# Optimization experiments

Measured on AMD Instinct MI355X. Metric: run time of the kernel, lower is better.

Reference implementation:

```python
import jax, jax.numpy as jnp
import numpy as np

B, T, F, H = 4, 2048, 512, 8
DK = F // H


def setup_inputs() -> dict:
    key = jax.random.key(0)
    ks = jax.random.split(key, 12)
    s = 1.0 / np.sqrt(F)
    return {
        "query": jax.random.normal(ks[0], (B, T, F), jnp.float32),
        "key": jax.random.normal(ks[1], (B, T, F), jnp.float32),
        "value": jax.random.normal(ks[2], (B, T, F), jnp.float32),
        "attn_mask": jax.random.randint(ks[3], (B, 1, T), 0, 2, jnp.int32),
        "Wq": jax.random.uniform(ks[4], (F, F), jnp.float32, -s, s),
        "bq": jax.random.uniform(ks[5], (F,), jnp.float32, -s, s),
        "Wk": jax.random.uniform(ks[6], (F, F), jnp.float32, -s, s),
        "bk": jax.random.uniform(ks[7], (F,), jnp.float32, -s, s),
        "Wv": jax.random.uniform(ks[8], (F, F), jnp.float32, -s, s),
        "bv": jax.random.uniform(ks[9], (F,), jnp.float32, -s, s),
        "Wo": jax.random.uniform(ks[10], (F, F), jnp.float32, -s, s),
        "bo": jax.random.uniform(ks[11], (F,), jnp.float32, -s, s),
    }


def reference(query, key, value, attn_mask, Wq, bq, Wk, bk, Wv, bv, Wo, bo):
    b = query.shape[0]
    # QKV projections -> (b, h, t, d_k)
    q = (query @ Wq.T + bq).reshape(b, -1, H, DK).transpose(0, 2, 1, 3)
    k = (key @ Wk.T + bk).reshape(b, -1, H, DK).transpose(0, 2, 1, 3)
    v = (value @ Wv.T + bv).reshape(b, -1, H, DK).transpose(0, 2, 1, 3)
    scores = jnp.einsum("bhqd,bhkd->bhqk", q, k) / np.sqrt(DK)
    # mask (b,1,t2) -> (b,1,1,t2); masked where mask == 0
    m = (attn_mask[:, None, :, :] == 0)
    min_val = jnp.finfo(scores.dtype).min
    scores = jnp.where(m, min_val, scores)
    attn = jnp.where(m, 0.0, jax.nn.softmax(scores, axis=-1))
    # dropout is identity in eval mode
    x = jnp.einsum("bhqk,bhkd->bhqd", attn, v)
    x = x.transpose(0, 2, 1, 3).reshape(b, -1, H * DK)
    return x @ Wo.T + bo
```

## Files before the change

### kernel.cpp

```cpp
#include <hip/hip_runtime.h>
#include <hip/hip_bf16.h>
#include <stdint.h>

#define B_ 4
#define T_ 2048
#define F_ 512
#define H_ 8
#define DK_ 64
#define BT_ (B_*T_)

typedef short bf16x8 __attribute__((ext_vector_type(8)));
typedef short s16x4 __attribute__((ext_vector_type(4)));
typedef float f32x4 __attribute__((ext_vector_type(4)));
typedef float f32x16 __attribute__((ext_vector_type(16)));

__device__ __forceinline__ unsigned short f2bf(float f) {
  union { float f; unsigned u; } v; v.f = f;
  return (unsigned short)((v.u + 0x7fffu + ((v.u >> 16) & 1u)) >> 16);
}

__device__ __forceinline__ unsigned cvtpk(float lo, float hi) {
  unsigned w;
  asm("v_cvt_pk_bf16_f32 %0, %1, %2" : "=v"(w) : "v"(lo), "v"(hi));
  return w;
}

__device__ __forceinline__ void gload_lds16(const void* g, void* l) {
  __builtin_amdgcn_global_load_lds((const __attribute__((address_space(1))) void*)g,
                                   (__attribute__((address_space(3))) void*)l, 16, 0, 0);
}

__global__ void convert_scan(const float* __restrict__ wq, const float* __restrict__ wk,
                             const float* __restrict__ wv, const float* __restrict__ wo,
                             const int* __restrict__ mask,
                             unsigned short* __restrict__ dst, int* __restrict__ invidx,
                             int* __restrict__ nbuf) {
  const int seg = blockIdx.y;
  const int tid = threadIdx.x;
  if (seg == 4) {
    if (blockIdx.x >= 4) return;
    const int b = blockIdx.x;
    __shared__ int cnt[256];
    const int base = b * T_ + tid * 8;
    int4 a = *(const int4*)(mask + base);
    int4 d = *(const int4*)(mask + base + 4);
    int m[8] = {a.x, a.y, a.z, a.w, d.x, d.y, d.z, d.w};
    int c = 0;
#pragma unroll
    for (int i = 0; i < 8; ++i) c += (m[i] != 0);
    cnt[tid] = c;
    __syncthreads();
    for (int off = 1; off < 256; off <<= 1) {
      int v = (tid >= off) ? cnt[tid - off] : 0;
      __syncthreads();
      cnt[tid] += v;
      __syncthreads();
    }
    int excl = cnt[tid] - c;
#pragma unroll
    for (int i = 0; i < 8; ++i)
      if (m[i]) { invidx[b * T_ + excl] = tid * 8 + i; ++excl; }
    if (tid == 255) nbuf[b] = cnt[255];
    return;
  }
  const float* src = seg == 0 ? wq : (seg == 1 ? wk : (seg == 2 ? wv : wo));
  unsigned short* out = dst + (size_t)seg * F_ * F_;
  const int idx = (blockIdx.x * 256 + tid) * 8;
  float4 a = *(const float4*)(src + idx);
  float4 b = *(const float4*)(src + idx + 4);
  union { unsigned w[4]; bf16x8 v; } t;
  t.w[0] = cvtpk(a.x, a.y); t.w[1] = cvtpk(a.z, a.w);
  t.w[2] = cvtpk(b.x, b.y); t.w[3] = cvtpk(b.z, b.w);
  *(bf16x8*)(out + idx) = t.v;
}

__global__ __launch_bounds__(256, 3) void gemm_qkv(
    const float* __restrict__ qin, const float* __restrict__ kin, const float* __restrict__ vin,
    const unsigned short* __restrict__ Wbase,
    const float* __restrict__ bq, const float* __restrict__ bk, const float* __restrict__ bv,
    const int* __restrict__ invidx, const int* __restrict__ nbuf,
    unsigned short* __restrict__ projq, unsigned short* __restrict__ kc,
    unsigned short* __restrict__ vt, float qscale) {
  const int id0 = blockIdx.x;
  const int id = (id0 & 7) * 96 + (id0 >> 3);
  const int p = id >> 8, l = id & 255;
  const int tid = threadIdx.x;
  const int wid = tid >> 6, lane = tid & 63;
  const int lr = lane & 15, lg = lane >> 4;
  const int wr = wid >> 1, wc = wid & 1;
  const int n0 = (l & 3) * 128;

  const float* Af;
  const float* bias;
  float sc = 1.0f;
  int obase, j0 = 0, b = 0, nb = T_;
  if (p == 0) {
    obase = (l >> 2) * 128;
    Af = qin; bias = bq; sc = qscale;
  } else {
    b = l >> 6;
    j0 = ((l >> 2) & 15) * 128;
    nb = nbuf[b];
    if (j0 >= ((nb + 63) & ~63)) return;
    obase = b * T_ + j0;
    Af = (p == 1) ? kin : vin;
    bias = (p == 1) ? bk : bv;
  }
  const unsigned short* W = Wbase + (size_t)p * F_ * F_;

  __shared__ __align__(16) unsigned short As[128 * 64];
  __shared__ __align__(16) unsigned short Bs[128 * 64];

  int srcrow[4];
#pragma unroll
  for (int i = 0; i < 4; ++i) {
    const int r = (i * 256 + tid) >> 3;
    if (p == 0) srcrow[i] = obase + r;
    else {
      int j = j0 + r;
      if (j >= nb) j = nb - 1;
      srcrow[i] = b * T_ + invidx[b * T_ + j];
    }
  }

  float4 aR[4][2];
  auto loadA = [&](int k0) {
#pragma unroll
    for (int i = 0; i < 4; ++i) {
      const int s = (i * 256 + tid) & 7;
      const float* sp = Af + (size_t)srcrow[i] * F_ + k0 + s * 8;
      aR[i][0] = *(const float4*)sp;
      aR[i][1] = *(const float4*)(sp + 4);
    }
  };
  auto writeA = [&]() {
#pragma unroll
    for (int i = 0; i < 4; ++i) {
      const int ch = i * 256 + tid;
      const int r = ch >> 3, s = ch & 7;
      union { unsigned w[4]; bf16x8 v; } t;
      t.w[0] = cvtpk(aR[i][0].x, aR[i][0].y); t.w[1] = cvtpk(aR[i][0].z, aR[i][0].w);
      t.w[2] = cvtpk(aR[i][1].x, aR[i][1].y); t.w[3] = cvtpk(aR[i][1].z, aR[i][1].w);
      *(bf16x8*)&As[r * 64 + ((s ^ (r & 7)) * 8)] = t.v;
    }
  };
  auto stageB = [&](int k0) {
#pragma unroll
    for (int i = 0; i < 4; ++i) {
      const int ch = i * 256 + tid;
      const int r = ch >> 3, s = ch & 7;
      gload_lds16(W + (size_t)(n0 + r) * F_ + k0 + ((s ^ (r & 7)) * 8),
                  &Bs[(i * 256 + wid * 64) * 8]);
    }
  };

  f32x4 acc[4][4] = {};
  loadA(0);
  for (int k0 = 0; k0 < F_; k0 += 64) {
    stageB(k0);
    writeA();
    __syncthreads();
    if (k0 + 64 < F_) loadA(k0 + 64);

#pragma unroll
    for (int kk = 0; kk < 2; ++kk) {
      bf16x8 af[4], bf[4];
      const int slotA = (kk * 4 + lg) ^ (lr & 7);
#pragma unroll
      for (int m = 0; m < 4; ++m)
        af[m] = *(const bf16x8*)&As[(wr * 64 + m * 16 + lr) * 64 + slotA * 8];
#pragma unroll
      for (int n = 0; n < 4; ++n)
        bf[n] = *(const bf16x8*)&Bs[(wc * 64 + n * 16 + lr) * 64 + slotA * 8];
#pragma unroll
      for (int m = 0; m < 4; ++m)
#pragma unroll
        for (int n = 0; n < 4; ++n)
          acc[m][n] = __builtin_amdgcn_mfma_f32_16x16x32_bf16(af[m], bf[n], acc[m][n], 0, 0, 0);
    }
    __syncthreads();
  }

  if (p == 2) {
#pragma unroll
    for (int n = 0; n < 4; ++n) {
      const int col = n0 + wc * 64 + n * 16 + lr;
      const float bvv = bias[col];
      unsigned short* vrow = vt + ((size_t)(b * 8 + (col >> 6)) * 64 + (col & 63)) * T_;
#pragma unroll
      for (int m = 0; m < 4; ++m) {
        const int kv = j0 + wr * 64 + m * 16 + lg * 4;
        union { unsigned short u[4]; s16x4 v; } ov;
#pragma unroll
        for (int j = 0; j < 4; ++j) ov.u[j] = f2bf(acc[m][n][j] + bvv);
        *(s16x4*)(vrow + kv) = ov.v;
      }
    }
  } else {
    unsigned short* outp = (p == 0) ? projq : kc;
#pragma unroll
    for (int n = 0; n < 4; ++n) {
      const int col = n0 + wc * 64 + n * 16 + lr;
      const float bvv = bias[col];
#pragma unroll
      for (int m = 0; m < 4; ++m) {
        const int rbase = obase + wr * 64 + m * 16 + lg * 4;
#pragma unroll
        for (int j = 0; j < 4; ++j)
          outp[(size_t)(rbase + j) * F_ + col] = f2bf((acc[m][n][j] + bvv) * sc);
      }
    }
  }
}

__global__ __launch_bounds__(256, 3) void gemm_out(
    const unsigned short* __restrict__ Abf, const unsigned short* __restrict__ W,
    const float* __restrict__ bias, float* __restrict__ outf) {
  const int id0 = blockIdx.x;
  const int l = (id0 & 7) * 64 + (id0 >> 3);
  const int m0 = (l >> 2) * 64, n0 = (l & 3) * 128;
  const int tid = threadIdx.x;
  const int wid = tid >> 6, lane = tid & 63;
  const int lr = lane & 15, lg = lane >> 4;
  const int wr = wid >> 1, wc = wid & 1;

  __shared__ __align__(16) unsigned short As[64 * 64];
  __shared__ __align__(16) unsigned short Bs[128 * 64];

  auto stage = [&](int k0) {
#pragma unroll
    for (int i = 0; i < 2; ++i) {
      const int ch = i * 256 + tid;
      const int r = ch >> 3, s = ch & 7;
      gload_lds16(Abf + (size_t)(m0 + r) * F_ + k0 + ((s ^ (r & 7)) * 8),
                  &As[(i * 256 + wid * 64) * 8]);
    }
#pragma unroll
    for (int i = 0; i < 4; ++i) {
      const int ch = i * 256 + tid;
      const int r = ch >> 3, s = ch & 7;
      gload_lds16(W + (size_t)(n0 + r) * F_ + k0 + ((s ^ (r & 7)) * 8),
                  &Bs[(i * 256 + wid * 64) * 8]);
    }
  };

  f32x4 acc[2][4] = {};
  for (int k0 = 0; k0 < F_; k0 += 64) {
    stage(k0);
    __syncthreads();
#pragma unroll
    for (int kk = 0; kk < 2; ++kk) {
      bf16x8 af[2], bf[4];
      const int slotA = (kk * 4 + lg) ^ (lr & 7);
#pragma unroll
      for (int m = 0; m < 2; ++m)
        af[m] = *(const bf16x8*)&As[(wr * 32 + m * 16 + lr) * 64 + slotA * 8];
#pragma unroll
      for (int n = 0; n < 4; ++n)
        bf[n] = *(const bf16x8*)&Bs[(wc * 64 + n * 16 + lr) * 64 + slotA * 8];
#pragma unroll
      for (int m = 0; m < 2; ++m)
#pragma unroll
        for (int n = 0; n < 4; ++n)
          acc[m][n] = __builtin_amdgcn_mfma_f32_16x16x32_bf16(af[m], bf[n], acc[m][n], 0, 0, 0);
    }
    __syncthreads();
  }

#pragma unroll
  for (int n = 0; n < 4; ++n) {
    const int col = n0 + wc * 64 + n * 16 + lr;
    const float bvv = bias[col];
#pragma unroll
    for (int m = 0; m < 2; ++m) {
      const int rbase = m0 + wr * 32 + m * 16 + lg * 4;
#pragma unroll
      for (int j = 0; j < 4; ++j)
        outf[(size_t)(rbase + j) * F_ + col] = acc[m][n][j] + bvv;
    }
  }
}

__global__ __launch_bounds__(256, 2) void attn_kernel(
    const unsigned short* __restrict__ Qp,
    const unsigned short* __restrict__ Kp,
    const unsigned short* __restrict__ Vt,
    const int* __restrict__ nbuf,
    unsigned short* __restrict__ X) {
  const int tid = threadIdx.x, wid = tid >> 6, lane = tid & 63;
  const int la = lane & 31, hi = lane >> 5;
  const int id = blockIdx.x;
  const int swz = (id & 7) * 64 + (id >> 3);
  const int bh = swz >> 4, qb = swz & 15;
  const int b = bh >> 3, h = bh & 7;
  const int qrow = qb * 128 + wid * 32 + la;
  const int nb = nbuf[b];
  const int nt = (nb + 127) >> 7;

  __shared__ __align__(16) unsigned short Ks[2][128 * 64];
  __shared__ __align__(16) unsigned short Vs[2][64 * 128];

  bf16x8 qf[4];
#pragma unroll
  for (int kk = 0; kk < 4; ++kk)
    qf[kk] = *(const bf16x8*)(Qp + (size_t)(b * T_ + qrow) * F_ + h * DK_ + kk * 16 + hi * 8);

  f32x16 oacc[2] = {};
  float lrun = 0.0f;

  auto stage = [&](int buf, int kv0) {
#pragma unroll
    for (int i = 0; i < 4; ++i) {
      const int ch = i * 256 + tid;
      const int r = ch >> 3, s = ch & 7;
      gload_lds16(Kp + (size_t)(b * T_ + kv0 + r) * F_ + h * DK_ + ((s ^ (r & 7)) * 8),
                  &Ks[buf][(i * 256 + wid * 64) * 8]);
      const int d = ch >> 4, s2 = ch & 15;
      gload_lds16(Vt + ((size_t)bh * DK_ + d) * T_ + kv0 + ((s2 ^ (d & 15)) * 8),
                  &Vs[buf][(i * 256 + wid * 64) * 8]);
    }
  };

  if (nt > 0) {
    stage(0, 0);
    __syncthreads();

    for (int t = 0; t < nt; ++t) {
      const int cur = t & 1;
      const int kv0 = t * 128;
      if (t < nt - 1) stage(cur ^ 1, kv0 + 128);

      f32x16 sb[4];
      __builtin_amdgcn_s_setprio(1);
#pragma unroll
      for (int n = 0; n < 4; ++n) {
        bf16x8 kf[4];
#pragma unroll
        for (int kk = 0; kk < 4; ++kk)
          kf[kk] = *(const bf16x8*)&Ks[cur][(n * 32 + la) * 64 + ((((kk << 1) | hi) ^ (la & 7)) * 8)];
        f32x16 s = {};
#pragma unroll
        for (int kk = 0; kk < 4; ++kk)
          s = __builtin_amdgcn_mfma_f32_32x32x16_bf16(kf[kk], qf[kk], s, 0, 0, 0);
        sb[n] = s;
      }
      __builtin_amdgcn_s_setprio(0);

      if (kv0 + 128 > nb) {
        const int kvb = kv0 + 4 * hi;
#pragma unroll
        for (int n = 0; n < 4; ++n)
#pragma unroll
          for (int r = 0; r < 16; ++r) {
            const int kv = kvb + n * 32 + (r & 3) + 8 * (r >> 2);
            if (kv >= nb) sb[n][r] = -__builtin_inff();
          }
      }
#pragma unroll
      for (int n = 0; n < 4; ++n)
#pragma unroll
        for (int r = 0; r < 16; ++r)
          sb[n][r] = __builtin_amdgcn_exp2f(sb[n][r]);

      float sm[16];
#pragma unroll
      for (int r = 0; r < 16; ++r)
        sm[r] = (sb[0][r] + sb[1][r]) + (sb[2][r] + sb[3][r]);
#pragma unroll
      for (int st = 8; st > 0; st >>= 1)
#pragma unroll
        for (int r = 0; r < st; ++r) sm[r] += sm[r + st];
      lrun += sm[0] + __shfl_xor(sm[0], 32, 64);

      unsigned lowr[4][2][2], uppr[4][2][2];
#pragma unroll
      for (int n = 0; n < 4; ++n)
#pragma unroll
        for (int gg = 0; gg < 2; ++gg)
#pragma unroll
          for (int hh = 0; hh < 2; ++hh) {
            unsigned xE = cvtpk(sb[n][4 * (2 * gg) + 2 * hh], sb[n][4 * (2 * gg) + 2 * hh + 1]);
            unsigned xO = cvtpk(sb[n][4 * (2 * gg + 1) + 2 * hh], sb[n][4 * (2 * gg + 1) + 2 * hh + 1]);
            asm("v_permlane32_swap_b32 %0, %1" : "+v"(xE), "+v"(xO));
            lowr[n][gg][hh] = xE;
            uppr[n][gg][hh] = xO;
          }

#pragma unroll
      for (int kt = 0; kt < 8; ++kt) {
        const int n = kt >> 1, gg = kt & 1;
        union { unsigned w[4]; bf16x8 v; } pf;
        pf.w[0] = lowr[n][gg][0]; pf.w[1] = lowr[n][gg][1];
        pf.w[2] = uppr[n][gg][0]; pf.w[3] = uppr[n][gg][1];
        __builtin_amdgcn_s_setprio(1);
#pragma unroll
        for (int m = 0; m < 2; ++m) {
          const int d = m * 32 + la;
          bf16x8 vfr = *(const bf16x8*)&Vs[cur][d * 128 + ((((kt << 1) | hi) ^ (d & 15)) * 8)];
          oacc[m] = __builtin_amdgcn_mfma_f32_32x32x16_bf16(vfr, pf.v, oacc[m], 0, 0, 0);
        }
        __builtin_amdgcn_s_setprio(0);
      }
      __syncthreads();
    }
  }

  const float inv = 1.0f / fmaxf(lrun, 1e-37f);
#pragma unroll
  for (int m = 0; m < 2; ++m)
#pragma unroll
    for (int g = 0; g < 4; ++g) {
      union { unsigned short u[4]; s16x4 v; } ov;
#pragma unroll
      for (int j = 0; j < 4; ++j) ov.u[j] = f2bf(oacc[m][4 * g + j] * inv);
      *(s16x4*)(X + (size_t)(b * T_ + qrow) * F_ + h * DK_ + m * 32 + 8 * g + 4 * hi) = ov.v;
    }
}

extern "C" void kernel_launch(void* const* d_in, const int* in_sizes, int n_in,
                              void* d_out, int out_size, void* d_ws, size_t ws_size,
                              hipStream_t stream) {
  const float* q  = (const float*)d_in[0];
  const float* k  = (const float*)d_in[1];
  const float* v  = (const float*)d_in[2];
  const int* mask = (const int*)d_in[3];
  const float* Wq = (const float*)d_in[4];
  const float* bq = (const float*)d_in[5];
  const float* Wk = (const float*)d_in[6];
  const float* bk = (const float*)d_in[7];
  const float* Wv = (const float*)d_in[8];
  const float* bv = (const float*)d_in[9];
  const float* Wo = (const float*)d_in[10];
  const float* bo = (const float*)d_in[11];
  float* out = (float*)d_out;

  unsigned short* ws = (unsigned short*)d_ws;
  unsigned short* wts   = ws;
  unsigned short* projq = wts + (size_t)4 * F_ * F_;
  unsigned short* kc    = projq + (size_t)BT_ * F_;
  unsigned short* vt    = kc + (size_t)BT_ * F_;
  unsigned short* xbuf  = vt + (size_t)BT_ * F_;
  int* invidx  = (int*)(xbuf + (size_t)BT_ * F_);
  int* nbuf    = invidx + BT_;

  const float kQScale = 0.18033688011112042f;

  convert_scan<<<dim3(128, 5, 1), 256, 0, stream>>>(
      Wq, Wk, Wv, Wo, mask, wts, invidx, nbuf);
  gemm_qkv<<<dim3(768, 1, 1), 256, 0, stream>>>(
      q, k, v, wts, bq, bk, bv, invidx, nbuf, projq, kc, vt, kQScale);
  attn_kernel<<<dim3(512, 1, 1), 256, 0, stream>>>(
      projq, kc, vt, nbuf, xbuf);
  gemm_out<<<dim3(512, 1, 1), 256, 0, stream>>>(
      xbuf, wts + (size_t)3 * F_ * F_, bo, out);
}
```

Measured before the change: 70.18 us.

## Use 512-thread attention blocks with triple-buffered KV and MFMA row sums

The attention kernel now runs 256 blocks of 8 waves, each covering 256 query rows, so every staged K/V tile is shared by twice as many waves. K/V staging moves from double to triple buffering with explicit vmcnt waits and one barrier per iteration, letting loads run two tiles ahead. The softmax denominator is now computed by an extra MFMA against a ones vector instead of VALU reductions and a shuffle. The cost is fewer blocks, more LDS per block (about 96KB), one extra MFMA per k-step, and reliance on hand-counted vmcnt values for correctness.

After: 68.68 us. 2.1% less time.

```diff
diff --git a/kernel.cpp b/kernel.cpp
--- a/kernel.cpp
+++ b/kernel.cpp
@@ -281,7 +281,7 @@
   }
 }
 
-__global__ __launch_bounds__(256, 2) void attn_kernel(
+__global__ __launch_bounds__(512, 1) void attn_kernel(
     const unsigned short* __restrict__ Qp,
     const unsigned short* __restrict__ Kp,
     const unsigned short* __restrict__ Vt,
@@ -290,45 +290,56 @@
   const int tid = threadIdx.x, wid = tid >> 6, lane = tid & 63;
   const int la = lane & 31, hi = lane >> 5;
   const int id = blockIdx.x;
-  const int swz = (id & 7) * 64 + (id >> 3);
-  const int bh = swz >> 4, qb = swz & 15;
+  const int swz = (id & 7) * 32 + (id >> 3);
+  const int bh = swz >> 3, qb = swz & 7;
   const int b = bh >> 3, h = bh & 7;
-  const int qrow = qb * 128 + wid * 32 + la;
+  const int qrow = qb * 256 + wid * 32 + la;
   const int nb = nbuf[b];
   const int nt = (nb + 127) >> 7;
 
-  __shared__ __align__(16) unsigned short Ks[2][128 * 64];
-  __shared__ __align__(16) unsigned short Vs[2][64 * 128];
+  __shared__ __align__(16) unsigned short Ks[3][128 * 64];
+  __shared__ __align__(16) unsigned short Vs[3][64 * 128];
 
   bf16x8 qf[4];
 #pragma unroll
   for (int kk = 0; kk < 4; ++kk)
     qf[kk] = *(const bf16x8*)(Qp + (size_t)(b * T_ + qrow) * F_ + h * DK_ + kk * 16 + hi * 8);
 
+  union { unsigned short u[8]; bf16x8 v; } ones;
+#pragma unroll
+  for (int j = 0; j < 8; ++j) ones.u[j] = 0x3F80;
+
   f32x16 oacc[2] = {};
-  float lrun = 0.0f;
+  f32x16 dacc = {};
 
   auto stage = [&](int buf, int kv0) {
 #pragma unroll
-    for (int i = 0; i < 4; ++i) {
-      const int ch = i * 256 + tid;
+    for (int i = 0; i < 2; ++i) {
+      const int ch = i * 512 + tid;
       const int r = ch >> 3, s = ch & 7;
       gload_lds16(Kp + (size_t)(b * T_ + kv0 + r) * F_ + h * DK_ + ((s ^ (r & 7)) * 8),
-                  &Ks[buf][(i * 256 + wid * 64) * 8]);
+                  &Ks[buf][(i * 512 + wid * 64) * 8]);
       const int d = ch >> 4, s2 = ch & 15;
       gload_lds16(Vt + ((size_t)bh * DK_ + d) * T_ + kv0 + ((s2 ^ (d & 15)) * 8),
-                  &Vs[buf][(i * 256 + wid * 64) * 8]);
+                  &Vs[buf][(i * 512 + wid * 64) * 8]);
     }
   };
 
   if (nt > 0) {
     stage(0, 0);
-    __syncthreads();
-
+    if (nt > 1) stage(1, 128);
+
+    int cur = 0;
     for (int t = 0; t < nt; ++t) {
-      const int cur = t & 1;
+      if (t + 1 < nt) asm volatile("s_waitcnt vmcnt(4)" ::: "memory");
+      else            asm volatile("s_waitcnt vmcnt(0)" ::: "memory");
+      __builtin_amdgcn_s_barrier();
+      __builtin_amdgcn_sched_barrier(0);
+      if (t + 2 < nt) {
+        int nxt = cur + 2; if (nxt >= 3) nxt -= 3;
+        stage(nxt, (t + 2) * 128);
+      }
       const int kv0 = t * 128;
-      if (t < nt - 1) stage(cur ^ 1, kv0 + 128);
 
       f32x16 sb[4];
       __builtin_amdgcn_s_setprio(1);
@@ -361,16 +372,6 @@
 #pragma unroll
         for (int r = 0; r < 16; ++r)
           sb[n][r] = __builtin_amdgcn_exp2f(sb[n][r]);
-
-      float sm[16];
-#pragma unroll
-      for (int r = 0; r < 16; ++r)
-        sm[r] = (sb[0][r] + sb[1][r]) + (sb[2][r] + sb[3][r]);
-#pragma unroll
-      for (int st = 8; st > 0; st >>= 1)
-#pragma unroll
-        for (int r = 0; r < st; ++r) sm[r] += sm[r + st];
-      lrun += sm[0] + __shfl_xor(sm[0], 32, 64);
 
       unsigned lowr[4][2][2], uppr[4][2][2];
 #pragma unroll
@@ -393,6 +394,7 @@
         pf.w[0] = lowr[n][gg][0]; pf.w[1] = lowr[n][gg][1];
         pf.w[2] = uppr[n][gg][0]; pf.w[3] = uppr[n][gg][1];
         __builtin_amdgcn_s_setprio(1);
+        dacc = __builtin_amdgcn_mfma_f32_32x32x16_bf16(ones.v, pf.v, dacc, 0, 0, 0);
 #pragma unroll
         for (int m = 0; m < 2; ++m) {
           const int d = m * 32 + la;
@@ -401,11 +403,12 @@
         }
         __builtin_amdgcn_s_setprio(0);
       }
-      __syncthreads();
-    }
-  }
-
-  const float inv = 1.0f / fmaxf(lrun, 1e-37f);
+
+      cur = (cur + 1 < 3) ? cur + 1 : 0;
+    }
+  }
+
+  const float inv = 1.0f / fmaxf(dacc[0], 1e-37f);
 #pragma unroll
   for (int m = 0; m < 2; ++m)
 #pragma unroll
@@ -449,7 +452,7 @@
       Wq, Wk, Wv, Wo, mask, wts, invidx, nbuf);
   gemm_qkv<<<dim3(768, 1, 1), 256, 0, stream>>>(
       q, k, v, wts, bq, bk, bv, invidx, nbuf, projq, kc, vt, kQScale);
-  attn_kernel<<<dim3(512, 1, 1), 256, 0, stream>>>(
+  attn_kernel<<<dim3(256, 1, 1), 512, 0, stream>>>(
       projq, kc, vt, nbuf, xbuf);
   gemm_out<<<dim3(512, 1, 1), 256, 0, stream>>>(
       xbuf, wts + (size_t)3 * F_ * F_, bo, out);
```
